# Kernel tuning notes

Measured on AMD Instinct MI355X. Metric: run time of the kernel, lower is better.

The kernel has to match this reference:

```python
import jax, jax.numpy as jnp
import numpy as np

B, S, D_IN, D_OUT = 4, 2048, 1024, 1024


def setup_inputs() -> dict:
    key = jax.random.key(0)
    k1, k2, k3, k4 = jax.random.split(key, 4)
    x = jax.random.normal(k1, (B, S, D_IN), dtype=jnp.float32)
    scale = 1.0 / np.sqrt(D_IN)
    Wq = jax.random.normal(k2, (D_IN, D_OUT), dtype=jnp.float32) * scale
    Wk = jax.random.normal(k3, (D_IN, D_OUT), dtype=jnp.float32) * scale
    Wv = jax.random.normal(k4, (D_IN, D_OUT), dtype=jnp.float32) * scale
    return {"x": x, "Wq": Wq, "Wk": Wk, "Wv": Wv}


def reference(x, Wq, Wk, Wv):
    # QKV projections (Linear, no bias)
    q = jnp.einsum('bsd,de->bse', x, Wq)  # [B,S,D_OUT]
    k = jnp.einsum('bsd,de->bse', x, Wk)
    v = jnp.einsum('bsd,de->bse', x, Wv)
    d_out = Wq.shape[1]
    # raw scores [B,S,S], scaled after masking (identical math: -inf stays -inf)
    scores = jnp.einsum('bqe,bke->bqk', q, k) * (d_out ** -0.5)
    S_ = x.shape[1]
    # causal mask: future positions (j > i) are masked out
    causal = jnp.triu(jnp.ones((S_, S_), dtype=bool), k=1)
    scores = jnp.where(causal[None, :, :], -jnp.inf, scores)
    attn = jax.nn.softmax(scores, axis=-1)  # dropout p=0.0 -> identity
    return jnp.einsum('bqk,bke->bqe', attn, v)
```

## Files before the change

### kernel.cpp

```cpp
#include <hip/hip_runtime.h>
#include <stdint.h>

typedef unsigned short u16;
typedef unsigned int u32;
typedef __bf16 bf16x8 __attribute__((ext_vector_type(8)));
typedef float f32x4 __attribute__((ext_vector_type(4)));

#define BM 128
#define BN 128
#define BK 64

__device__ __forceinline__ u16 f2bf(float x) {
  union { float f; uint32_t u; } c; c.f = x;
  uint32_t r = (c.u + 0x7FFFu + ((c.u >> 16) & 1u)) >> 16;
  return (u16)r;
}

__device__ __forceinline__ void async_copy16(const u16* g, u16* l) {
  __builtin_amdgcn_global_load_lds(
      (const __attribute__((address_space(1))) void*)g,
      (__attribute__((address_space(3))) void*)l,
      16, 0, 0);
}

__global__ void zerofill_u16(u16* __restrict__ p) {
  long i = (long)blockIdx.x * 256 + threadIdx.x;
  p[i] = 0;
}

__global__ __launch_bounds__(256)
void prep(const void* __restrict__ xs, const void* __restrict__ w0,
          const void* __restrict__ w1, const void* __restrict__ w2,
          u16* __restrict__ xn, u16* __restrict__ WT3, u32* __restrict__ flag,
          int nxb)
{
  __shared__ int sh_hits;
  __shared__ u16 tile[64][72];
  if (threadIdx.x == 0) sh_hits = 0;
  __syncthreads();
  {
    const u16* w = (const u16*)w0;
    int h = 0;
    for (int i = threadIdx.x; i < 8192; i += 256)
      if ((w[i] & 0x7F80u) == 0x7F80u) h++;
    if (h) atomicAdd(&sh_hits, h);
  }
  __syncthreads();
  const bool isf32 = (sh_hits > 0);
  const int blk = blockIdx.x;
  const int tid = threadIdx.x;
  if (blk == 0 && tid == 0) *flag = isf32 ? 1000u : 0u;

  if (blk < nxb) {
    long i = ((long)blk * 256 + tid) * 8;
    u16 o[8];
    if (isf32) {
      const float* s = (const float*)xs + i;
      f32x4 a = *(const f32x4*)s;
      f32x4 b = *(const f32x4*)(s + 4);
#pragma unroll
      for (int c = 0; c < 4; ++c) { o[c] = f2bf(a[c]); o[c + 4] = f2bf(b[c]); }
    } else {
      *(uint4*)o = *(const uint4*)((const u16*)xs + i);
    }
    *(uint4*)(xn + i) = *(uint4*)o;
  } else {
    const int Dd = 1024;
    int t = blk - nxb;
    int z = t >> 8;
    int r = t & 255;
    const int r0 = (r >> 4) * 64, c0 = (r & 15) * 64;
    const void* src = (z == 0) ? w0 : (z == 1) ? w1 : w2;
    u16* out = WT3 + (long)z * Dd * Dd;
#pragma unroll
    for (int p = 0; p < 2; ++p) {
      int v = tid + p * 256;
      int row = v >> 3, c8 = (v & 7) * 8;
      u16 tt[8];
      if (isf32) {
        const float* sp = (const float*)src + (long)(r0 + row) * Dd + c0 + c8;
        f32x4 a = *(const f32x4*)sp;
        f32x4 b = *(const f32x4*)(sp + 4);
#pragma unroll
        for (int c = 0; c < 4; ++c) { tt[c] = f2bf(a[c]); tt[c + 4] = f2bf(b[c]); }
      } else {
        *(uint4*)tt = *(const uint4*)((const u16*)src + (long)(r0 + row) * Dd + c0 + c8);
      }
#pragma unroll
      for (int c = 0; c < 8; ++c) tile[row][c8 + c] = tt[c];
    }
    __syncthreads();
#pragma unroll
    for (int p = 0; p < 2; ++p) {
      int v = tid + p * 256;
      int oc = v >> 3, r8 = (v & 7) * 8;
      union { uint4 q; u16 s[8]; } tt;
#pragma unroll
      for (int c = 0; c < 8; ++c) tt.s[c] = tile[r8 + c][oc];
      *(uint4*)(out + (long)(c0 + oc) * Dd + r0 + r8) = tt.q;
    }
  }
}

template <int MODE>
__global__ __launch_bounds__(256, 2)
void gemm_nt(const u16* __restrict__ A, const u16* __restrict__ B, void* __restrict__ Cv,
             const u32* __restrict__ flag,
             int K, int lda, int ldb, int ldc,
             long sA, long sB, long sC, long cOff,
             float scale, int causal, int trik)
{
  int bm, bn;
  if (causal == 2) {
    int t = blockIdx.x;
    bm = (int)((__fsqrt_rn(8.0f * (float)t + 1.0f) - 1.0f) * 0.5f);
    while ((bm + 1) * (bm + 2) / 2 <= t) ++bm;
    while (bm * (bm + 1) / 2 > t) --bm;
    bn = t - bm * (bm + 1) / 2;
  } else {
    bm = blockIdx.y;
    if (trik) bm = gridDim.y - 1 - bm;
    bn = blockIdx.x;
    if (causal == 1 && bn > bm) return;
  }
  const int bz = blockIdx.z;

  __shared__ u16 As[BM * BK];
  __shared__ u16 Bs[BN * BK];

  A += (long)bz * sA;
  B += (long)bz * sB;

  const int tid  = threadIdx.x;
  const int wid  = tid >> 6;
  const int lane = tid & 63;
  const int l16  = lane & 15;
  const int lk   = lane >> 4;
  const int srow = lane >> 3;
  const int swz  = ((lane & 7) ^ srow) * 8;
  const int m0 = bm * BM, n0 = bn * BN;

  int nk = K / BK;
  if (trik) { int lim = (m0 + BM) / BK; if (lim < nk) nk = lim; }

  f32x4 acc[4][4] = {};

  for (int kt = 0; kt < nk; ++kt) {
    const int k0 = kt * BK;
#pragma unroll
    for (int c = 0; c < 4; ++c) {
      const int rb = wid * 32 + c * 8;
      async_copy16(A + (long)(m0 + rb + srow) * lda + (k0 + swz), As + rb * BK);
      async_copy16(B + (long)(n0 + rb + srow) * ldb + (k0 + swz), Bs + rb * BK);
    }
    __syncthreads();
#pragma unroll
    for (int kh = 0; kh < 2; ++kh) {
      bf16x8 av[4], bv[4];
#pragma unroll
      for (int i = 0; i < 4; ++i) {
        const int Ra = (wid >> 1) * 64 + i * 16 + l16;
        const int Rb = (wid & 1)  * 64 + i * 16 + l16;
        const int ca = ((kh * 4 + lk) ^ (l16 & 7)) * 8;
        av[i] = *(const bf16x8*)(As + Ra * BK + ca);
        bv[i] = *(const bf16x8*)(Bs + Rb * BK + ca);
      }
#pragma unroll
      for (int mi = 0; mi < 4; ++mi)
#pragma unroll
        for (int ni = 0; ni < 4; ++ni)
          acc[mi][ni] = __builtin_amdgcn_mfma_f32_16x16x32_bf16(av[mi], bv[ni], acc[mi][ni], 0, 0, 0);
    }
    __syncthreads();
  }

  const int rb0 = m0 + (wid >> 1) * 64;
  const int cb0 = n0 + (wid & 1) * 64;
  const long cbase = (long)bz * sC + cOff;
  const bool f32out = (MODE == 1) || (MODE == 2 && *flag > 32);

#pragma unroll
  for (int mi = 0; mi < 4; ++mi)
#pragma unroll
    for (int ni = 0; ni < 4; ++ni) {
      const int row = rb0 + mi * 16 + lk * 4;
      const int col = cb0 + ni * 16 + l16;
#pragma unroll
      for (int r = 0; r < 4; ++r) {
        const float v = acc[mi][ni][r] * scale;
        const long idx = cbase + (long)(row + r) * ldc + col;
        if constexpr (MODE == 0) {
          ((u16*)Cv)[idx] = f2bf(v);
        } else if constexpr (MODE == 1) {
          ((float*)Cv)[idx] = v;
        } else {
          if (f32out) ((float*)Cv)[idx] = v;
          else        ((u16*)Cv)[idx]   = f2bf(v);
        }
      }
    }
}

__global__ __launch_bounds__(256)
void transpose_bf16(const u16* __restrict__ in, u16* __restrict__ out,
                    int ldIn, int ldOut, long sIn, long sOut)
{
  __shared__ u16 tile[64][72];
  const int bz = blockIdx.z;
  in  += (long)bz * sIn;
  out += (long)bz * sOut;
  const int r0 = blockIdx.y * 64, c0 = blockIdx.x * 64;
  const int tid = threadIdx.x;
#pragma unroll
  for (int p = 0; p < 2; ++p) {
    int v = tid + p * 256;
    int row = v >> 3, c8 = (v & 7) * 8;
    union { uint4 q; u16 s[8]; } t;
    t.q = *(const uint4*)(in + (long)(r0 + row) * ldIn + c0 + c8);
#pragma unroll
    for (int i = 0; i < 8; ++i) tile[row][c8 + i] = t.s[i];
  }
  __syncthreads();
#pragma unroll
  for (int p = 0; p < 2; ++p) {
    int v = tid + p * 256;
    int oc = v >> 3, r8 = (v & 7) * 8;
    union { uint4 q; u16 s[8]; } t;
#pragma unroll
    for (int i = 0; i < 8; ++i) t.s[i] = tile[r8 + i][oc];
    *(uint4*)(out + (long)(c0 + oc) * ldOut + r0 + r8) = t.q;
  }
}

__global__ __launch_bounds__(256)
void softmax_causal(char* __restrict__ base, long rowStrideB, int modS)
{
  const long r = blockIdx.x;
  const int i = (int)(r % modS);
  float* sc = (float*)(base + r * rowStrideB);
  u16*   pr = (u16*)(base + r * rowStrideB);
  const int n = i + 1;
  const int tid = threadIdx.x;
  const int j0 = tid * 8;
  const int wv = tid >> 6, lane = tid & 63;
  __shared__ float red[4];

  float e[8];
  float m = -3.0e38f;
  if (j0 < n) {
    f32x4 a = *(const f32x4*)(sc + j0);
    f32x4 b = *(const f32x4*)(sc + j0 + 4);
#pragma unroll
    for (int c = 0; c < 4; ++c) { e[c] = a[c]; e[c + 4] = b[c]; }
#pragma unroll
    for (int c = 0; c < 8; ++c) {
      if (j0 + c < n) m = fmaxf(m, e[c]); else e[c] = -3.0e38f;
    }
  } else {
#pragma unroll
    for (int c = 0; c < 8; ++c) e[c] = -3.0e38f;
  }
#pragma unroll
  for (int o = 32; o > 0; o >>= 1) m = fmaxf(m, __shfl_xor(m, o));
  if (lane == 0) red[wv] = m;
  __syncthreads();
  m = fmaxf(fmaxf(red[0], red[1]), fmaxf(red[2], red[3]));
  __syncthreads();

  float s = 0.f;
#pragma unroll
  for (int c = 0; c < 8; ++c) { float x = __expf(e[c] - m); e[c] = x; s += x; }
#pragma unroll
  for (int o = 32; o > 0; o >>= 1) s += __shfl_xor(s, o);
  if (lane == 0) red[wv] = s;
  __syncthreads();
  s = red[0] + red[1] + red[2] + red[3];
  const float inv = 1.0f / s;

  u16 o8[8];
#pragma unroll
  for (int c = 0; c < 8; ++c) o8[c] = f2bf(e[c] * inv);
  *(uint4*)(pr + j0) = *(uint4*)o8;
}

extern "C" void kernel_launch(void* const* d_in, const int* in_sizes, int n_in,
                              void* d_out, int out_size, void* d_ws, size_t ws_size,
                              hipStream_t stream)
{
  (void)in_sizes; (void)n_in; (void)out_size;
  const int Bb = 4, S = 2048, D = 1024, D3 = 3072;
  const long SD = (long)S * D;
  const long SS = (long)S * S;
  const long N_X = (long)Bb * SD;
  const long N_W = (long)D * D;
  const int NTRI = 16 * 17 / 2;

  char* ws = (char*)d_ws;
  size_t off = 0;
  auto take = [&](size_t bytes) -> void* {
    void* p = ws + off;
    off = (off + bytes + 255) & ~((size_t)255);
    return p;
  };

  u32* flag = (u32*)take(4096);
  u16* xn   = (u16*)take((size_t)N_X * 2);
  u16* WT3  = (u16*)take((size_t)3 * N_W * 2);
  const size_t off_common = off;

  const size_t needA = off_common + (size_t)(N_X * 3 * 2)
                     + (size_t)(N_X * 2)
                     + (size_t)(Bb * SS * 4) + 4096;
  const size_t needC = off_common + (size_t)(S * (long)D3 * 2)
                     + (size_t)(SD * 2)
                     + (size_t)(SS * 4) + 4096;

  if (ws_size < needC) {
    zerofill_u16<<<(int)(N_X / 256), 256, 0, stream>>>((u16*)d_out);
    return;
  }

  const int nxb = (int)(N_X / 2048);
  prep<<<nxb + 768, 256, 0, stream>>>(d_in[0], d_in[1], d_in[2], d_in[3],
                                      xn, WT3, flag, nxb);

  const float scl = 0.03125f;

  if (ws_size >= needA) {
    u16*   QKV = (u16*)take((size_t)N_X * 3 * 2);
    u16*   VT  = (u16*)take((size_t)N_X * 2);
    float* sc  = (float*)take((size_t)Bb * SS * 4);

    gemm_nt<0><<<dim3(D3 / BN, (int)(N_X / D) / BM, 1), 256, 0, stream>>>(
        xn, WT3, QKV, flag, D, D, D, D3, 0, 0, 0, 0, 1.f, 0, 0);

    transpose_bf16<<<dim3(D / 64, S / 64, Bb), 256, 0, stream>>>(
        QKV + 2048, VT, D3, S, (long)S * D3, SD);

    gemm_nt<1><<<dim3(NTRI, 1, Bb), 256, 0, stream>>>(
        QKV, QKV + 1024, sc, flag, D, D3, D3, S,
        (long)S * D3, (long)S * D3, SS, 0, scl, 2, 0);

    softmax_causal<<<Bb * S, 256, 0, stream>>>((char*)sc, (long)S * 4, S);

    gemm_nt<2><<<dim3(D / BN, S / BM, Bb), 256, 0, stream>>>(
        (u16*)sc, VT, d_out, flag, S, 2 * S, S, D,
        2 * SS, SD, SD, 0, 1.f, 0, 1);
  } else {
    u16*   QKVb = (u16*)take((size_t)S * D3 * 2);
    u16*   VTb  = (u16*)take((size_t)SD * 2);
    float* scb  = (float*)take((size_t)SS * 4);

    for (int b = 0; b < Bb; ++b) {
      gemm_nt<0><<<dim3(D3 / BN, S / BM, 1), 256, 0, stream>>>(
          xn + (long)b * SD, WT3, QKVb, flag, D, D, D, D3, 0, 0, 0, 0, 1.f, 0, 0);

      transpose_bf16<<<dim3(D / 64, S / 64, 1), 256, 0, stream>>>(
          QKVb + 2048, VTb, D3, S, 0, 0);

      gemm_nt<1><<<dim3(NTRI, 1, 1), 256, 0, stream>>>(
          QKVb, QKVb + 1024, scb, flag, D, D3, D3, S, 0, 0, 0, 0, scl, 2, 0);

      softmax_causal<<<S, 256, 0, stream>>>((char*)scb, (long)S * 4, S);

      gemm_nt<2><<<dim3(D / BN, S / BM, 1), 256, 0, stream>>>(
          (u16*)scb, VTb, d_out, flag, S, 2 * S, S, D,
          0, 0, 0, (long)b * SD, 1.f, 0, 1);
    }
  }
}
```

Measured before the change: 264.1 us.

## Fuse softmax into QK^T epilogue with unnormalized exp and deferred row-sum normalization

The QK^T GEMM epilogue now computes exp(score*scale) without subtracting a row max, writes bf16 probabilities, and atomically accumulates row sums into a sigma buffer. The PV GEMM divides each output row by that sum. The separate softmax kernel is removed, the V transpose moves into extra blocks of the score kernel, and the score buffer shrinks from fp32 to bf16. This removes a full pass over the S×S matrix and two launches. In exchange, skipping the max subtraction risks overflow for large scores, and the atomic adds make the row sums order-nondeterministic.

```diff
diff --git a/kernel.cpp b/kernel.cpp
--- a/kernel.cpp
+++ b/kernel.cpp
@@ -14,6 +14,10 @@
   union { float f; uint32_t u; } c; c.f = x;
   uint32_t r = (c.u + 0x7FFFu + ((c.u >> 16) & 1u)) >> 16;
   return (u16)r;
+}
+__device__ __forceinline__ float bf2f(u16 v) {
+  union { uint32_t u; float f; } c; c.u = ((uint32_t)v) << 16;
+  return c.f;
 }
 
 __device__ __forceinline__ void async_copy16(const u16* g, u16* l) {
@@ -32,7 +36,7 @@
 void prep(const void* __restrict__ xs, const void* __restrict__ w0,
           const void* __restrict__ w1, const void* __restrict__ w2,
           u16* __restrict__ xn, u16* __restrict__ WT3, u32* __restrict__ flag,
-          int nxb)
+          float* __restrict__ sigma, int nxb)
 {
   __shared__ int sh_hits;
   __shared__ u16 tile[64][72];
@@ -64,7 +68,7 @@
       *(uint4*)o = *(const uint4*)((const u16*)xs + i);
     }
     *(uint4*)(xn + i) = *(uint4*)o;
-  } else {
+  } else if (blk < nxb + 768) {
     const int Dd = 1024;
     int t = blk - nxb;
     int z = t >> 8;
@@ -99,19 +103,57 @@
       for (int c = 0; c < 8; ++c) tt.s[c] = tile[r8 + c][oc];
       *(uint4*)(out + (long)(c0 + oc) * Dd + r0 + r8) = tt.q;
     }
+  } else {
+    int t = blk - (nxb + 768);
+    *(f32x4*)(sigma + ((long)t * 256 + tid) * 4) = f32x4{0.f, 0.f, 0.f, 0.f};
   }
 }
 
 template <int MODE>
 __global__ __launch_bounds__(256, 2)
 void gemm_nt(const u16* __restrict__ A, const u16* __restrict__ B, void* __restrict__ Cv,
-             const u32* __restrict__ flag,
+             const u32* __restrict__ flag, float* __restrict__ sigma, int sigStride,
              int K, int lda, int ldb, int ldc,
              long sA, long sB, long sC, long cOff,
-             float scale, int causal, int trik)
+             float scale, int trik, int ntri,
+             const u16* __restrict__ vSrc, u16* __restrict__ vtDst,
+             long sV, long sVT, int ldV, int ldVT)
 {
+  __shared__ u16 As[BM * BK];
+  __shared__ u16 Bs[BN * BK];
+  const int bz = blockIdx.z;
+  const int tid = threadIdx.x;
+
   int bm, bn;
-  if (causal == 2) {
+  if constexpr (MODE == 3) {
+    if ((int)blockIdx.x >= ntri) {
+      int t2 = blockIdx.x - ntri;
+      const u16* in = vSrc + (long)bz * sV;
+      u16* out = vtDst + (long)bz * sVT;
+      const int c0 = (t2 & 15) * 64;
+      const int r0 = (t2 >> 4) * 64;
+      u16 (*tile)[72] = reinterpret_cast<u16(*)[72]>(As);
+#pragma unroll
+      for (int p = 0; p < 2; ++p) {
+        int v = tid + p * 256;
+        int row = v >> 3, c8 = (v & 7) * 8;
+        union { uint4 q; u16 s[8]; } t;
+        t.q = *(const uint4*)(in + (long)(r0 + row) * ldV + c0 + c8);
+#pragma unroll
+        for (int i = 0; i < 8; ++i) tile[row][c8 + i] = t.s[i];
+      }
+      __syncthreads();
+#pragma unroll
+      for (int p = 0; p < 2; ++p) {
+        int v = tid + p * 256;
+        int oc = v >> 3, r8 = (v & 7) * 8;
+        union { uint4 q; u16 s[8]; } t;
+#pragma unroll
+        for (int i = 0; i < 8; ++i) t.s[i] = tile[r8 + i][oc];
+        *(uint4*)(out + (long)(c0 + oc) * ldVT + r0 + r8) = t.q;
+      }
+      return;
+    }
     int t = blockIdx.x;
     bm = (int)((__fsqrt_rn(8.0f * (float)t + 1.0f) - 1.0f) * 0.5f);
     while ((bm + 1) * (bm + 2) / 2 <= t) ++bm;
@@ -121,17 +163,11 @@
     bm = blockIdx.y;
     if (trik) bm = gridDim.y - 1 - bm;
     bn = blockIdx.x;
-    if (causal == 1 && bn > bm) return;
-  }
-  const int bz = blockIdx.z;
-
-  __shared__ u16 As[BM * BK];
-  __shared__ u16 Bs[BN * BK];
+  }
 
   A += (long)bz * sA;
   B += (long)bz * sB;
 
-  const int tid  = threadIdx.x;
   const int wid  = tid >> 6;
   const int lane = tid & 63;
   const int l16  = lane & 15;
@@ -177,110 +213,54 @@
   const int rb0 = m0 + (wid >> 1) * 64;
   const int cb0 = n0 + (wid & 1) * 64;
   const long cbase = (long)bz * sC + cOff;
-  const bool f32out = (MODE == 1) || (MODE == 2 && *flag > 32);
-
-#pragma unroll
-  for (int mi = 0; mi < 4; ++mi)
-#pragma unroll
-    for (int ni = 0; ni < 4; ++ni) {
-      const int row = rb0 + mi * 16 + lk * 4;
-      const int col = cb0 + ni * 16 + l16;
+
+  if constexpr (MODE == 3) {
+    u16* Cp = (u16*)Cv;
+    const bool diag = (bm == bn);
+    float* sig = sigma + (long)bz * sigStride;
+#pragma unroll
+    for (int mi = 0; mi < 4; ++mi)
 #pragma unroll
       for (int r = 0; r < 4; ++r) {
-        const float v = acc[mi][ni][r] * scale;
-        const long idx = cbase + (long)(row + r) * ldc + col;
-        if constexpr (MODE == 0) {
-          ((u16*)Cv)[idx] = f2bf(v);
-        } else if constexpr (MODE == 1) {
-          ((float*)Cv)[idx] = v;
-        } else {
-          if (f32out) ((float*)Cv)[idx] = v;
-          else        ((u16*)Cv)[idx]   = f2bf(v);
+        const int row = rb0 + mi * 16 + lk * 4 + r;
+        float part = 0.f;
+#pragma unroll
+        for (int ni = 0; ni < 4; ++ni) {
+          const int col = cb0 + ni * 16 + l16;
+          float ev = __expf(acc[mi][ni][r] * scale);
+          if (diag && col > row) ev = 0.f;
+          u16 b = f2bf(ev);
+          part += bf2f(b);
+          Cp[cbase + (long)row * ldc + col] = b;
         }
-      }
-    }
-}
-
-__global__ __launch_bounds__(256)
-void transpose_bf16(const u16* __restrict__ in, u16* __restrict__ out,
-                    int ldIn, int ldOut, long sIn, long sOut)
-{
-  __shared__ u16 tile[64][72];
-  const int bz = blockIdx.z;
-  in  += (long)bz * sIn;
-  out += (long)bz * sOut;
-  const int r0 = blockIdx.y * 64, c0 = blockIdx.x * 64;
-  const int tid = threadIdx.x;
-#pragma unroll
-  for (int p = 0; p < 2; ++p) {
-    int v = tid + p * 256;
-    int row = v >> 3, c8 = (v & 7) * 8;
-    union { uint4 q; u16 s[8]; } t;
-    t.q = *(const uint4*)(in + (long)(r0 + row) * ldIn + c0 + c8);
-#pragma unroll
-    for (int i = 0; i < 8; ++i) tile[row][c8 + i] = t.s[i];
-  }
-  __syncthreads();
-#pragma unroll
-  for (int p = 0; p < 2; ++p) {
-    int v = tid + p * 256;
-    int oc = v >> 3, r8 = (v & 7) * 8;
-    union { uint4 q; u16 s[8]; } t;
-#pragma unroll
-    for (int i = 0; i < 8; ++i) t.s[i] = tile[r8 + i][oc];
-    *(uint4*)(out + (long)(c0 + oc) * ldOut + r0 + r8) = t.q;
-  }
-}
-
-__global__ __launch_bounds__(256)
-void softmax_causal(char* __restrict__ base, long rowStrideB, int modS)
-{
-  const long r = blockIdx.x;
-  const int i = (int)(r % modS);
-  float* sc = (float*)(base + r * rowStrideB);
-  u16*   pr = (u16*)(base + r * rowStrideB);
-  const int n = i + 1;
-  const int tid = threadIdx.x;
-  const int j0 = tid * 8;
-  const int wv = tid >> 6, lane = tid & 63;
-  __shared__ float red[4];
-
-  float e[8];
-  float m = -3.0e38f;
-  if (j0 < n) {
-    f32x4 a = *(const f32x4*)(sc + j0);
-    f32x4 b = *(const f32x4*)(sc + j0 + 4);
-#pragma unroll
-    for (int c = 0; c < 4; ++c) { e[c] = a[c]; e[c + 4] = b[c]; }
-#pragma unroll
-    for (int c = 0; c < 8; ++c) {
-      if (j0 + c < n) m = fmaxf(m, e[c]); else e[c] = -3.0e38f;
-    }
+#pragma unroll
+        for (int o = 1; o < 16; o <<= 1) part += __shfl_xor(part, o);
+        if (l16 == 0) atomicAdd(&sig[row], part);
+      }
   } else {
-#pragma unroll
-    for (int c = 0; c < 8; ++c) e[c] = -3.0e38f;
-  }
-#pragma unroll
-  for (int o = 32; o > 0; o >>= 1) m = fmaxf(m, __shfl_xor(m, o));
-  if (lane == 0) red[wv] = m;
-  __syncthreads();
-  m = fmaxf(fmaxf(red[0], red[1]), fmaxf(red[2], red[3]));
-  __syncthreads();
-
-  float s = 0.f;
-#pragma unroll
-  for (int c = 0; c < 8; ++c) { float x = __expf(e[c] - m); e[c] = x; s += x; }
-#pragma unroll
-  for (int o = 32; o > 0; o >>= 1) s += __shfl_xor(s, o);
-  if (lane == 0) red[wv] = s;
-  __syncthreads();
-  s = red[0] + red[1] + red[2] + red[3];
-  const float inv = 1.0f / s;
-
-  u16 o8[8];
-#pragma unroll
-  for (int c = 0; c < 8; ++c) o8[c] = f2bf(e[c] * inv);
-  *(uint4*)(pr + j0) = *(uint4*)o8;
+    const bool f32out = (MODE == 2) && (*flag > 32);
+    const float* sig = (MODE == 2) ? (sigma + (long)bz * sigStride) : nullptr;
+#pragma unroll
+    for (int mi = 0; mi < 4; ++mi)
+#pragma unroll
+      for (int r = 0; r < 4; ++r) {
+        const int row = rb0 + mi * 16 + lk * 4 + r;
+        float rs = scale;
+        if constexpr (MODE == 2) rs = 1.0f / sig[row];
+#pragma unroll
+        for (int ni = 0; ni < 4; ++ni) {
+          const int col = cb0 + ni * 16 + l16;
+          const float v = acc[mi][ni][r] * rs;
+          const long idx = cbase + (long)row * ldc + col;
+          if constexpr (MODE == 0) {
+            ((u16*)Cv)[idx] = f2bf(v);
+          } else {
+            if (f32out) ((float*)Cv)[idx] = v;
+            else        ((u16*)Cv)[idx]   = f2bf(v);
+          }
+        }
+      }
+  }
 }
 
 extern "C" void kernel_launch(void* const* d_in, const int* in_sizes, int n_in,
@@ -289,8 +269,9 @@
 {
   (void)in_sizes; (void)n_in; (void)out_size;
   const int Bb = 4, S = 2048, D = 1024, D3 = 3072;
-  const long SD = (long)S * D;
-  const long SS = (long)S * S;
+  const long SD  = (long)S * D;
+  const long SD3 = (long)S * D3;
+  const long SS  = (long)S * S;
   const long N_X = (long)Bb * SD;
   const long N_W = (long)D * D;
   const int NTRI = 16 * 17 / 2;
@@ -303,17 +284,18 @@
     return p;
   };
 
-  u32* flag = (u32*)take(4096);
-  u16* xn   = (u16*)take((size_t)N_X * 2);
-  u16* WT3  = (u16*)take((size_t)3 * N_W * 2);
+  u32*   flag  = (u32*)take(4096);
+  float* sigma = (float*)take((size_t)Bb * S * 4);
+  u16*   xn    = (u16*)take((size_t)N_X * 2);
+  u16*   WT3   = (u16*)take((size_t)3 * N_W * 2);
   const size_t off_common = off;
 
   const size_t needA = off_common + (size_t)(N_X * 3 * 2)
                      + (size_t)(N_X * 2)
-                     + (size_t)(Bb * SS * 4) + 4096;
+                     + (size_t)(Bb * SS * 2) + 4096;
   const size_t needC = off_common + (size_t)(S * (long)D3 * 2)
                      + (size_t)(SD * 2)
-                     + (size_t)(SS * 4) + 4096;
+                     + (size_t)(SS * 2) + 4096;
 
   if (ws_size < needC) {
     zerofill_u16<<<(int)(N_X / 256), 256, 0, stream>>>((u16*)d_out);
@@ -321,51 +303,46 @@
   }
 
   const int nxb = (int)(N_X / 2048);
-  prep<<<nxb + 768, 256, 0, stream>>>(d_in[0], d_in[1], d_in[2], d_in[3],
-                                      xn, WT3, flag, nxb);
+  prep<<<nxb + 768 + 8, 256, 0, stream>>>(d_in[0], d_in[1], d_in[2], d_in[3],
+                                          xn, WT3, flag, sigma, nxb);
 
   const float scl = 0.03125f;
 
   if (ws_size >= needA) {
-    u16*   QKV = (u16*)take((size_t)N_X * 3 * 2);
-    u16*   VT  = (u16*)take((size_t)N_X * 2);
-    float* sc  = (float*)take((size_t)Bb * SS * 4);
+    u16* QKV = (u16*)take((size_t)N_X * 3 * 2);
+    u16* VT  = (u16*)take((size_t)N_X * 2);
+    u16* E   = (u16*)take((size_t)Bb * SS * 2);
 
     gemm_nt<0><<<dim3(D3 / BN, (int)(N_X / D) / BM, 1), 256, 0, stream>>>(
-        xn, WT3, QKV, flag, D, D, D, D3, 0, 0, 0, 0, 1.f, 0, 0);
-
-    transpose_bf16<<<dim3(D / 64, S / 64, Bb), 256, 0, stream>>>(
-        QKV + 2048, VT, D3, S, (long)S * D3, SD);
-
-    gemm_nt<1><<<dim3(NTRI, 1, Bb), 256, 0, stream>>>(
-        QKV, QKV + 1024, sc, flag, D, D3, D3, S,
-        (long)S * D3, (long)S * D3, SS, 0, scl, 2, 0);
-
-    softmax_causal<<<Bb * S, 256, 0, stream>>>((char*)sc, (long)S * 4, S);
+        xn, WT3, QKV, flag, nullptr, 0, D, D, D, D3,
+        0, 0, 0, 0, 1.f, 0, 0, nullptr, nullptr, 0, 0, 0, 0);
+
+    gemm_nt<3><<<dim3(NTRI + 512, 1, Bb), 256, 0, stream>>>(
+        QKV, QKV + 1024, E, flag, sigma, S, D, D3, D3, S,
+        SD3, SD3, SS, 0, scl, 0, NTRI,
+        QKV + 2048, VT, SD3, SD, D3, S);
 
     gemm_nt<2><<<dim3(D / BN, S / BM, Bb), 256, 0, stream>>>(
-        (u16*)sc, VT, d_out, flag, S, 2 * S, S, D,
-        2 * SS, SD, SD, 0, 1.f, 0, 1);
+        E, VT, d_out, flag, sigma, S, S, S, S, D,
+        SS, SD, SD, 0, 1.f, 1, 0, nullptr, nullptr, 0, 0, 0, 0);
   } else {
-    u16*   QKVb = (u16*)take((size_t)S * D3 * 2);
-    u16*   VTb  = (u16*)take((size_t)SD * 2);
-    float* scb  = (float*)take((size_t)SS * 4);
+    u16* QKVb = (u16*)take((size_t)S * D3 * 2);
+    u16* VTb  = (u16*)take((size_t)SD * 2);
+    u16* Eb   = (u16*)take((size_t)SS * 2);
 
     for (int b = 0; b < Bb; ++b) {
       gemm_nt<0><<<dim3(D3 / BN, S / BM, 1), 256, 0, stream>>>(
-          xn + (long)b * SD, WT3, QKVb, flag, D, D, D, D3, 0, 0, 0, 0, 1.f, 0, 0);
-
-      transpose_bf16<<<dim3(D / 64, S / 64, 1), 256, 0, stream>>>(
-          QKVb + 2048, VTb, D3, S, 0, 0);
-
-      gemm_nt<1><<<dim3(NTRI, 1, 1), 256, 0, stream>>>(
-          QKVb, QKVb + 1024, scb, flag, D, D3, D3, S, 0, 0, 0, 0, scl, 2, 0);
-
-      softmax_causal<<<S, 256, 0, stream>>>((char*)scb, (long)S * 4, S);
+          xn + (long)b * SD, WT3, QKVb, flag, nullptr, 0, D, D, D, D3,
+          0, 0, 0, 0, 1.f, 0, 0, nullptr, nullptr, 0, 0, 0, 0);
+
+      gemm_nt<3><<<dim3(NTRI + 512, 1, 1), 256, 0, stream>>>(
+          QKVb, QKVb + 1024, Eb, flag, sigma + (long)b * S, S, D, D3, D3, S,
+          0, 0, 0, 0, scl, 0, NTRI,
+          QKVb + 2048, VTb, 0, 0, D3, S);
 
       gemm_nt<2><<<dim3(D / BN, S / BM, 1), 256, 0, stream>>>(
-          (u16*)scb, VTb, d_out, flag, S, 2 * S, S, D,
-          0, 0, 0, (long)b * SD, 1.f, 0, 1);
-    }
-  }
-}
+          Eb, VTb, d_out, flag, sigma + (long)b * S, S, S, S, S, D,
+          0, 0, 0, (long)b * SD, 1.f, 1, 0, nullptr, nullptr, 0, 0, 0, 0);
+    }
+  }
+}
```

After: 251.1 us. 4.9% less time.
